# Performance work log

Measured on AMD Instinct MI355X. Metric: run time of the kernel, lower is better.

The kernel has to match this reference:

```python
import jax, jax.numpy as jnp
import numpy as np

D_EMB, D_PROJ, N_HEADS, HIDDEN = 640, 256, 4, 128
HEAD_DIM = D_PROJ // N_HEADS
B = 65536
EPS = 1e-5


def setup_inputs() -> dict:
    key = jax.random.key(0)
    ks = jax.random.split(key, 14)
    def w(k, shape, fan_in):
        return (jax.random.normal(k, shape, jnp.float32) / np.sqrt(fan_in)).astype(jnp.float32)
    return {
        "global_diff": jax.random.normal(ks[0], (B, D_EMB), jnp.float32),
        "local_diff": jax.random.normal(ks[1], (B, D_EMB), jnp.float32),
        # global/local projections ([in, out] layout; math identical to torch Linear)
        "Wg": w(ks[2], (D_EMB, D_PROJ), D_EMB), "bg": jnp.zeros((D_PROJ,), jnp.float32),
        "Wl": w(ks[3], (D_EMB, D_PROJ), D_EMB), "bl": jnp.zeros((D_PROJ,), jnp.float32),
        # MultiheadAttention packed in-proj (q|k|v) and out-proj
        "W_in": w(ks[4], (D_PROJ, 3 * D_PROJ), D_PROJ), "b_in": jnp.zeros((3 * D_PROJ,), jnp.float32),
        "W_out": w(ks[5], (D_PROJ, D_PROJ), D_PROJ), "b_out": jnp.zeros((D_PROJ,), jnp.float32),
        # LayerNorm
        "gamma": jnp.ones((D_PROJ,), jnp.float32), "beta": jnp.zeros((D_PROJ,), jnp.float32),
        # MLP head
        "W1": w(ks[6], (D_PROJ, HIDDEN), D_PROJ), "b1": jnp.zeros((HIDDEN,), jnp.float32),
        "W2": w(ks[7], (HIDDEN, 1), HIDDEN), "b2": jnp.zeros((1,), jnp.float32),
    }


def reference(global_diff, local_diff, Wg, bg, Wl, bl, W_in, b_in, W_out, b_out,
              gamma, beta, W1, b1, W2, b2):
    # projections (eval mode: dropout inactive)
    g = global_diff @ Wg + bg              # [B, P] -- the single query token
    l = local_diff @ Wl + bl               # [B, P]
    kv = jnp.stack([g, l], axis=1)         # [B, 2, P]

    Wq, Wk, Wv = jnp.split(W_in, 3, axis=1)
    bq, bk, bv = jnp.split(b_in, 3)
    b = g.shape[0]
    q = (g @ Wq + bq).reshape(b, N_HEADS, HEAD_DIM)        # [B, H, d]
    k = (kv @ Wk + bk).reshape(b, 2, N_HEADS, HEAD_DIM)    # [B, 2, H, d]
    v = (kv @ Wv + bv).reshape(b, 2, N_HEADS, HEAD_DIM)

    scale = 1.0 / np.sqrt(HEAD_DIM)
    scores = jnp.einsum('bhd,bshd->bhs', q, k) * scale     # [B, H, 2]
    attn = jax.nn.softmax(scores, axis=-1)
    ctx = jnp.einsum('bhs,bshd->bhd', attn, v).reshape(b, D_PROJ)
    attended = ctx @ W_out + b_out                         # [B, P]

    # residual + LayerNorm (eps=1e-5, torch default)
    x = g + attended
    mu = jnp.mean(x, axis=-1, keepdims=True)
    var = jnp.mean(jnp.square(x - mu), axis=-1, keepdims=True)
    y = (x - mu) * jax.lax.rsqrt(var + EPS) * gamma + beta

    # MLP head: Linear -> exact GELU (torch default) -> Linear
    h = jax.nn.gelu(y @ W1 + b1, approximate=False)
    out = (h @ W2 + b2).squeeze(-1)                        # [B]
    return out
```

## Files before the change

### kernel.cpp

```cpp
#include <hip/hip_runtime.h>
#include <math.h>

typedef __attribute__((ext_vector_type(4))) float f32x4;
typedef __attribute__((ext_vector_type(8))) __bf16 bf16x8;

static constexpr int WG_OFF = 0;
static constexpr int WL_OFF = 163840;
static constexpr int WQ_OFF = 327680;
static constexpr int WK_OFF = 393216;
static constexpr int WV_OFF = 458752;
static constexpr int WO_OFF = 524288;
static constexpr int W1_OFF = 589824;
static constexpr int W_TOTAL = 622592;

__device__ __forceinline__ unsigned short f2bf(float f) {
  unsigned u = __builtin_bit_cast(unsigned, f);
  u += 0x7FFFu + ((u >> 16) & 1u);
  return (unsigned short)(u >> 16);
}

__device__ __forceinline__ f32x4 mfma16(bf16x8 a, bf16x8 b, f32x4 c) {
  return __builtin_amdgcn_mfma_f32_16x16x32_bf16(a, b, c, 0, 0, 0);
}
__device__ __forceinline__ f32x4 fzero4() {
  f32x4 v; v[0] = 0.f; v[1] = 0.f; v[2] = 0.f; v[3] = 0.f; return v;
}

__device__ __forceinline__ bf16x8 ldB(const unsigned short* __restrict__ ws, int fragIdx, int lane) {
  return *(const bf16x8*)(ws + (size_t)(fragIdx * 64 + lane) * 8);
}

template <int STRIDE>
__device__ __forceinline__ bf16x8 ldA(const char* s, int row, int kbyte) {
  return *(const bf16x8*)(s + row * STRIDE + (kbyte ^ ((row & 7) << 4)));
}

__device__ __forceinline__ void stC(char* s, int row, int col, float v) {
  *(__bf16*)(s + row * 512 + ((col * 2) ^ ((row & 7) << 4))) = (__bf16)v;
}
__device__ __forceinline__ float ldC(const char* s, int row, int col) {
  return (float)*(const __bf16*)(s + row * 512 + ((col * 2) ^ ((row & 7) << 4)));
}

__device__ __forceinline__ bf16x8 cvt8(float4 a, float4 b) {
  bf16x8 t;
  t[0] = (__bf16)a.x; t[1] = (__bf16)a.y; t[2] = (__bf16)a.z; t[3] = (__bf16)a.w;
  t[4] = (__bf16)b.x; t[5] = (__bf16)b.y; t[6] = (__bf16)b.z; t[7] = (__bf16)b.w;
  return t;
}

template <int N>
__device__ __forceinline__ void red16(float* v) {
#pragma unroll
  for (int m = 1; m < 16; m <<= 1) {
#pragma unroll
    for (int i = 0; i < N; ++i) v[i] += __shfl_xor(v[i], m);
  }
}

__device__ __forceinline__ void stageA32(const float* __restrict__ A, char* sA, int tid) {
#pragma unroll
  for (int i = 0; i < 5; ++i) {
    const int idx = i * 512 + tid;
    const int row = idx / 80;
    const int c8 = idx - row * 80;
    const float* ap = A + (size_t)idx * 8;
    float4 f0 = *(const float4*)ap;
    float4 f1 = *(const float4*)(ap + 4);
    *(bf16x8*)(sA + row * 1280 + ((c8 * 16) ^ ((row & 7) << 4))) = cvt8(f0, f1);
  }
}

__device__ __forceinline__ void proj640(const char* sA, const unsigned short* __restrict__ wsW,
                                        const float* __restrict__ bias, char* sDst,
                                        int f0, int lane) {
  const int l15 = lane & 15, kg4 = lane >> 4;
  f32x4 acc[2][2];
#pragma unroll
  for (int m = 0; m < 2; ++m)
#pragma unroll
    for (int n = 0; n < 2; ++n) acc[m][n] = fzero4();
#pragma unroll 2
  for (int kt = 0; kt < 20; ++kt) {
    bf16x8 b0 = ldB(wsW, kt * 16 + f0, lane);
    bf16x8 b1 = ldB(wsW, kt * 16 + f0 + 1, lane);
    const int kb = kt * 64 + kg4 * 16;
#pragma unroll
    for (int m = 0; m < 2; ++m) {
      bf16x8 a = ldA<1280>(sA, m * 16 + l15, kb);
      acc[m][0] = mfma16(a, b0, acc[m][0]);
      acc[m][1] = mfma16(a, b1, acc[m][1]);
    }
  }
#pragma unroll
  for (int n = 0; n < 2; ++n) {
    const int col = (f0 + n) * 16 + l15;
    const float bv = bias[col];
#pragma unroll
    for (int m = 0; m < 2; ++m)
#pragma unroll
      for (int r = 0; r < 4; ++r)
        stC(sDst, m * 16 + kg4 * 4 + r, col, acc[m][n][r] + bv);
  }
}

__device__ __forceinline__ void gemm256(const char* sA, const unsigned short* __restrict__ wsW,
                                        int f0, f32x4 (&acc)[2][2], int lane) {
  const int l15 = lane & 15, kg4 = lane >> 4;
#pragma unroll 2
  for (int kt = 0; kt < 8; ++kt) {
    bf16x8 b0 = ldB(wsW, kt * 16 + f0, lane);
    bf16x8 b1 = ldB(wsW, kt * 16 + f0 + 1, lane);
    const int kb = kt * 64 + kg4 * 16;
#pragma unroll
    for (int m = 0; m < 2; ++m) {
      bf16x8 a = ldA<512>(sA, m * 16 + l15, kb);
      acc[m][0] = mfma16(a, b0, acc[m][0]);
      acc[m][1] = mfma16(a, b1, acc[m][1]);
    }
  }
}

__device__ __forceinline__ void gemm256d(const char* sG, const char* sL,
                                         const unsigned short* __restrict__ wsW, int f0,
                                         f32x4 (&ag)[2][2], f32x4 (&al)[2][2], int lane) {
  const int l15 = lane & 15, kg4 = lane >> 4;
#pragma unroll 2
  for (int kt = 0; kt < 8; ++kt) {
    bf16x8 b0 = ldB(wsW, kt * 16 + f0, lane);
    bf16x8 b1 = ldB(wsW, kt * 16 + f0 + 1, lane);
    const int kb = kt * 64 + kg4 * 16;
#pragma unroll
    for (int m = 0; m < 2; ++m) {
      bf16x8 g = ldA<512>(sG, m * 16 + l15, kb);
      bf16x8 l = ldA<512>(sL, m * 16 + l15, kb);
      ag[m][0] = mfma16(g, b0, ag[m][0]);
      ag[m][1] = mfma16(g, b1, ag[m][1]);
      al[m][0] = mfma16(l, b0, al[m][0]);
      al[m][1] = mfma16(l, b1, al[m][1]);
    }
  }
}

__global__ void convert_w(const float* __restrict__ Wg, const float* __restrict__ Wl,
                          const float* __restrict__ Win, const float* __restrict__ Wout,
                          const float* __restrict__ W1, unsigned short* __restrict__ ws) {
  const int tid = blockIdx.x * 256 + threadIdx.x;
  if (tid >= W_TOTAL) return;
  const float* src;
  int stride, coloff, base, lognf;
  if (tid < WL_OFF)      { src = Wg;   stride = 256; coloff = 0;   base = WG_OFF; lognf = 4; }
  else if (tid < WQ_OFF) { src = Wl;   stride = 256; coloff = 0;   base = WL_OFF; lognf = 4; }
  else if (tid < WK_OFF) { src = Win;  stride = 768; coloff = 0;   base = WQ_OFF; lognf = 4; }
  else if (tid < WV_OFF) { src = Win;  stride = 768; coloff = 256; base = WK_OFF; lognf = 4; }
  else if (tid < WO_OFF) { src = Win;  stride = 768; coloff = 512; base = WV_OFF; lognf = 4; }
  else if (tid < W1_OFF) { src = Wout; stride = 256; coloff = 0;   base = WO_OFF; lognf = 4; }
  else                   { src = W1;   stride = 128; coloff = 0;   base = W1_OFF; lognf = 3; }
  const int idx = tid - base;
  const int j = idx & 7;
  const int lane = (idx >> 3) & 63;
  const int fl = idx >> 9;
  const int n = fl & ((1 << lognf) - 1);
  const int kt = fl >> lognf;
  const int k = kt * 32 + (lane >> 4) * 8 + j;
  const int col = coloff + n * 16 + (lane & 15);
  ws[tid] = f2bf(src[k * stride + col]);
}

__global__ __launch_bounds__(512)
__attribute__((amdgpu_waves_per_eu(4, 4)))
void dca_fused(
    const float* __restrict__ gdiff, const float* __restrict__ ldiff,
    const float* __restrict__ bg, const float* __restrict__ bl,
    const float* __restrict__ bin, const float* __restrict__ bout,
    const float* __restrict__ gamma, const float* __restrict__ beta,
    const float* __restrict__ b1, const float* __restrict__ W2,
    const float* __restrict__ b2, const unsigned short* __restrict__ wsw,
    float* __restrict__ out) {
  __shared__ __align__(16) char sMem[73728];
  char* sA = sMem;
  char* sG = sMem + 40960;
  char* sL = sMem + 57344;
  float* sSc = (float*)sMem;
  float* sLN = (float*)(sMem + 2048);
  float* sMu = (float*)(sMem + 4096);
  float* sPO = (float*)(sMem + 4352);
  char* sQ = sMem + 8192;

  const int tid = threadIdx.x;
  const int blk = blockIdx.x;
  const int lane = tid & 63, l15 = lane & 15, kg4 = lane >> 4;
  const int w = tid >> 6;
  const int f0 = w * 2;

  stageA32(gdiff + (size_t)blk * 32 * 640, sA, tid);
  __syncthreads();
  proj640(sA, wsw + WG_OFF, bg, sG, f0, lane);
  __syncthreads();
  stageA32(ldiff + (size_t)blk * 32 * 640, sA, tid);
  __syncthreads();
  proj640(sA, wsw + WL_OFF, bl, sL, f0, lane);
  __syncthreads();

  {
    f32x4 qa[2][2];
#pragma unroll
    for (int m = 0; m < 2; ++m) { qa[m][0] = fzero4(); qa[m][1] = fzero4(); }
    gemm256(sG, wsw + WQ_OFF, f0, qa, lane);
#pragma unroll
    for (int m = 0; m < 2; ++m) {
      bf16x8 t;
#pragma unroll
      for (int n = 0; n < 2; ++n) {
        const float bv = bin[(f0 + n) * 16 + l15];
#pragma unroll
        for (int r = 0; r < 4; ++r) t[n * 4 + r] = (__bf16)(qa[m][n][r] + bv);
      }
      *(bf16x8*)(sQ + m * 8192 + tid * 16) = t;
    }
  }

  float s[16];
  {
    f32x4 kg[2][2], kl[2][2];
#pragma unroll
    for (int m = 0; m < 2; ++m) {
      kg[m][0] = fzero4(); kg[m][1] = fzero4();
      kl[m][0] = fzero4(); kl[m][1] = fzero4();
    }
    gemm256d(sG, sL, wsw + WK_OFF, f0, kg, kl, lane);
#pragma unroll
    for (int m = 0; m < 2; ++m) {
      bf16x8 t = *(const bf16x8*)(sQ + m * 8192 + tid * 16);
#pragma unroll
      for (int r = 0; r < 4; ++r) {
        s[m * 4 + r] = (float)t[r] * kg[m][0][r] + (float)t[4 + r] * kg[m][1][r];
        s[8 + m * 4 + r] = (float)t[r] * kl[m][0][r] + (float)t[4 + r] * kl[m][1][r];
      }
    }
  }
  red16<16>(s);
  if (l15 < 2) {
#pragma unroll
    for (int r = 0; r < 4; ++r) {
      const int row = l15 * 16 + kg4 * 4 + r;
      sSc[(w * 32 + row) * 2 + 0] = s[l15 * 4 + r];
      sSc[(w * 32 + row) * 2 + 1] = s[8 + l15 * 4 + r];
    }
  }
  __syncthreads();
  float a1v[2][4];
  {
    const int pw = w ^ 1;
#pragma unroll
    for (int m = 0; m < 2; ++m)
#pragma unroll
      for (int r = 0; r < 4; ++r) {
        const int row = m * 16 + kg4 * 4 + r;
        const float t0 = s[m * 4 + r] + sSc[(pw * 32 + row) * 2 + 0];
        const float t1 = s[8 + m * 4 + r] + sSc[(pw * 32 + row) * 2 + 1];
        a1v[m][r] = 1.0f / (1.0f + expf((t0 - t1) * 0.125f));
      }
  }

  f32x4 ctx[2][2];
  {
    f32x4 vg[2][2], vl[2][2];
#pragma unroll
    for (int m = 0; m < 2; ++m) {
      vg[m][0] = fzero4(); vg[m][1] = fzero4();
      vl[m][0] = fzero4(); vl[m][1] = fzero4();
    }
    gemm256d(sG, sL, wsw + WV_OFF, f0, vg, vl, lane);
#pragma unroll
    for (int n = 0; n < 2; ++n) {
      const float bv = bin[512 + (f0 + n) * 16 + l15];
#pragma unroll
      for (int m = 0; m < 2; ++m)
#pragma unroll
        for (int r = 0; r < 4; ++r)
          ctx[m][n][r] = (1.0f - a1v[m][r]) * vg[m][n][r] + a1v[m][r] * vl[m][n][r] + bv;
    }
  }
  __syncthreads();
#pragma unroll
  for (int n = 0; n < 2; ++n) {
    const int col = (f0 + n) * 16 + l15;
#pragma unroll
    for (int m = 0; m < 2; ++m)
#pragma unroll
      for (int r = 0; r < 4; ++r)
        stC(sL, m * 16 + kg4 * 4 + r, col, ctx[m][n][r]);
  }
  __syncthreads();

  {
    f32x4 at[2][2];
#pragma unroll
    for (int m = 0; m < 2; ++m) { at[m][0] = fzero4(); at[m][1] = fzero4(); }
    gemm256(sL, wsw + WO_OFF, f0, at, lane);
    float st[16];
#pragma unroll
    for (int i = 0; i < 16; ++i) st[i] = 0.f;
#pragma unroll
    for (int n = 0; n < 2; ++n) {
      const int col = (f0 + n) * 16 + l15;
      const float bv = bout[col];
#pragma unroll
      for (int m = 0; m < 2; ++m)
#pragma unroll
        for (int r = 0; r < 4; ++r) {
          const int row = m * 16 + kg4 * 4 + r;
          const float x = at[m][n][r] + bv + ldC(sG, row, col);
          stC(sG, row, col, x);
          st[m * 4 + r] += x;
          st[8 + m * 4 + r] += x * x;
        }
    }
    red16<16>(st);
    if (l15 < 2) {
#pragma unroll
      for (int r = 0; r < 4; ++r) {
        const int row = l15 * 16 + kg4 * 4 + r;
        sLN[(w * 32 + row) * 2 + 0] = st[l15 * 4 + r];
        sLN[(w * 32 + row) * 2 + 1] = st[8 + l15 * 4 + r];
      }
    }
  }
  __syncthreads();
  if (tid < 64) {
    const int row = tid >> 1, j = tid & 1;
    float v = 0.f;
#pragma unroll
    for (int ww = 0; ww < 8; ++ww) v += sLN[(ww * 32 + row) * 2 + j];
    sMu[row * 2 + j] = v;
  }
  __syncthreads();
#pragma unroll
  for (int n = 0; n < 2; ++n) {
    const int col = (f0 + n) * 16 + l15;
    const float ga = gamma[col], be = beta[col];
#pragma unroll
    for (int m = 0; m < 2; ++m)
#pragma unroll
      for (int r = 0; r < 4; ++r) {
        const int row = m * 16 + kg4 * 4 + r;
        const float m_ = sMu[row * 2 + 0] * (1.0f / 256.0f);
        const float var = sMu[row * 2 + 1] * (1.0f / 256.0f) - m_ * m_;
        const float x = ldC(sG, row, col);
        stC(sG, row, col, (x - m_) * rsqrtf(var + 1e-5f) * ga + be);
      }
  }
  __syncthreads();

  f32x4 ha[2];
  ha[0] = fzero4();
  ha[1] = fzero4();
#pragma unroll 2
  for (int kt = 0; kt < 8; ++kt) {
    bf16x8 b = ldB(wsw + W1_OFF, kt * 8 + w, lane);
    const int kb = kt * 64 + kg4 * 16;
#pragma unroll
    for (int m = 0; m < 2; ++m) {
      bf16x8 a = ldA<512>(sG, m * 16 + l15, kb);
      ha[m] = mfma16(a, b, ha[m]);
    }
  }
  {
    const int colh = w * 16 + l15;
    const float bv1 = b1[colh], w2v = W2[colh];
    float o[8];
#pragma unroll
    for (int m = 0; m < 2; ++m)
#pragma unroll
      for (int r = 0; r < 4; ++r) {
        float hv = ha[m][r] + bv1;
        hv = 0.5f * hv * (1.0f + erff(hv * 0.70710678118654752f));
        o[m * 4 + r] = hv * w2v;
      }
    red16<8>(o);
    if (l15 < 2) {
#pragma unroll
      for (int r = 0; r < 4; ++r)
        sPO[w * 32 + l15 * 16 + kg4 * 4 + r] = o[l15 * 4 + r];
    }
  }
  __syncthreads();
  if (tid < 32) {
    float acc = b2[0];
#pragma unroll
    for (int ww = 0; ww < 8; ++ww) acc += sPO[ww * 32 + tid];
    out[(size_t)blk * 32 + tid] = acc;
  }
}

extern "C" void kernel_launch(void* const* d_in, const int* in_sizes, int n_in,
                              void* d_out, int out_size, void* d_ws, size_t ws_size,
                              hipStream_t stream) {
  (void)in_sizes; (void)n_in; (void)out_size; (void)ws_size;
  const float* gdiff = (const float*)d_in[0];
  const float* ldiff = (const float*)d_in[1];
  const float* Wg    = (const float*)d_in[2];
  const float* bg    = (const float*)d_in[3];
  const float* Wl    = (const float*)d_in[4];
  const float* bl    = (const float*)d_in[5];
  const float* Win   = (const float*)d_in[6];
  const float* bin   = (const float*)d_in[7];
  const float* Wout  = (const float*)d_in[8];
  const float* bout  = (const float*)d_in[9];
  const float* gamma = (const float*)d_in[10];
  const float* beta  = (const float*)d_in[11];
  const float* W1    = (const float*)d_in[12];
  const float* b1    = (const float*)d_in[13];
  const float* W2    = (const float*)d_in[14];
  const float* b2    = (const float*)d_in[15];
  unsigned short* ws = (unsigned short*)d_ws;
  float* out = (float*)d_out;

  convert_w<<<dim3((W_TOTAL + 255) / 256), dim3(256), 0, stream>>>(Wg, Wl, Win, Wout, W1, ws);
  dca_fused<<<dim3(2048), dim3(512), 0, stream>>>(gdiff, ldiff, bg, bl, bin, bout, gamma,
                                                  beta, b1, W2, b2,
                                                  (const unsigned short*)ws, out);
}
```

Baseline: 207.9 us.

## Process 64 rows per block with 16 waves each owning one column tile

Doubles the rows per workgroup from 32 to 64 and the threads from 512 to 1024. Each wave now owns a single 16-wide output column tile across four row tiles instead of two column tiles across two row tiles, so each weight fragment loaded from global memory is reused over more rows. Attention score and LayerNorm reductions are reworked into a two-level cross-wave reduction through shared memory. LDS use doubles to 144KB, which allows only one block per CU and may reduce latency hiding. The extra reduction pass adds barriers.

```diff
diff --git a/kernel.cpp b/kernel.cpp
--- a/kernel.cpp
+++ b/kernel.cpp
@@ -58,10 +58,10 @@
   }
 }
 
-__device__ __forceinline__ void stageA32(const float* __restrict__ A, char* sA, int tid) {
+__device__ __forceinline__ void stageA64(const float* __restrict__ A, char* sA, int tid) {
 #pragma unroll
   for (int i = 0; i < 5; ++i) {
-    const int idx = i * 512 + tid;
+    const int idx = i * 1024 + tid;
     const int row = idx / 80;
     const int c8 = idx - row * 80;
     const float* ap = A + (size_t)idx * 8;
@@ -71,73 +71,61 @@
   }
 }
 
-__device__ __forceinline__ void proj640(const char* sA, const unsigned short* __restrict__ wsW,
-                                        const float* __restrict__ bias, char* sDst,
-                                        int f0, int lane) {
+__device__ __forceinline__ void proj640w(const char* sA, const unsigned short* __restrict__ wsW,
+                                         const float* __restrict__ bias, char* sDst,
+                                         int w, int lane) {
   const int l15 = lane & 15, kg4 = lane >> 4;
-  f32x4 acc[2][2];
-#pragma unroll
-  for (int m = 0; m < 2; ++m)
-#pragma unroll
-    for (int n = 0; n < 2; ++n) acc[m][n] = fzero4();
+  f32x4 acc[4];
+#pragma unroll
+  for (int m = 0; m < 4; ++m) acc[m] = fzero4();
 #pragma unroll 2
   for (int kt = 0; kt < 20; ++kt) {
-    bf16x8 b0 = ldB(wsW, kt * 16 + f0, lane);
-    bf16x8 b1 = ldB(wsW, kt * 16 + f0 + 1, lane);
+    bf16x8 b = ldB(wsW, kt * 16 + w, lane);
     const int kb = kt * 64 + kg4 * 16;
 #pragma unroll
-    for (int m = 0; m < 2; ++m) {
+    for (int m = 0; m < 4; ++m) {
       bf16x8 a = ldA<1280>(sA, m * 16 + l15, kb);
-      acc[m][0] = mfma16(a, b0, acc[m][0]);
-      acc[m][1] = mfma16(a, b1, acc[m][1]);
-    }
-  }
-#pragma unroll
-  for (int n = 0; n < 2; ++n) {
-    const int col = (f0 + n) * 16 + l15;
-    const float bv = bias[col];
-#pragma unroll
-    for (int m = 0; m < 2; ++m)
-#pragma unroll
-      for (int r = 0; r < 4; ++r)
-        stC(sDst, m * 16 + kg4 * 4 + r, col, acc[m][n][r] + bv);
-  }
-}
-
-__device__ __forceinline__ void gemm256(const char* sA, const unsigned short* __restrict__ wsW,
-                                        int f0, f32x4 (&acc)[2][2], int lane) {
+      acc[m] = mfma16(a, b, acc[m]);
+    }
+  }
+  const int col = w * 16 + l15;
+  const float bv = bias[col];
+#pragma unroll
+  for (int m = 0; m < 4; ++m)
+#pragma unroll
+    for (int r = 0; r < 4; ++r)
+      stC(sDst, m * 16 + kg4 * 4 + r, col, acc[m][r] + bv);
+}
+
+__device__ __forceinline__ void gemm256w(const char* sA, const unsigned short* __restrict__ wsW,
+                                         int w, f32x4 (&acc)[4], int lane) {
   const int l15 = lane & 15, kg4 = lane >> 4;
 #pragma unroll 2
   for (int kt = 0; kt < 8; ++kt) {
-    bf16x8 b0 = ldB(wsW, kt * 16 + f0, lane);
-    bf16x8 b1 = ldB(wsW, kt * 16 + f0 + 1, lane);
+    bf16x8 b = ldB(wsW, kt * 16 + w, lane);
     const int kb = kt * 64 + kg4 * 16;
 #pragma unroll
-    for (int m = 0; m < 2; ++m) {
+    for (int m = 0; m < 4; ++m) {
       bf16x8 a = ldA<512>(sA, m * 16 + l15, kb);
-      acc[m][0] = mfma16(a, b0, acc[m][0]);
-      acc[m][1] = mfma16(a, b1, acc[m][1]);
-    }
-  }
-}
-
-__device__ __forceinline__ void gemm256d(const char* sG, const char* sL,
-                                         const unsigned short* __restrict__ wsW, int f0,
-                                         f32x4 (&ag)[2][2], f32x4 (&al)[2][2], int lane) {
+      acc[m] = mfma16(a, b, acc[m]);
+    }
+  }
+}
+
+__device__ __forceinline__ void gemm256dw(const char* sG, const char* sL,
+                                          const unsigned short* __restrict__ wsW, int w,
+                                          f32x4 (&ag)[4], f32x4 (&al)[4], int lane) {
   const int l15 = lane & 15, kg4 = lane >> 4;
 #pragma unroll 2
   for (int kt = 0; kt < 8; ++kt) {
-    bf16x8 b0 = ldB(wsW, kt * 16 + f0, lane);
-    bf16x8 b1 = ldB(wsW, kt * 16 + f0 + 1, lane);
+    bf16x8 b = ldB(wsW, kt * 16 + w, lane);
     const int kb = kt * 64 + kg4 * 16;
 #pragma unroll
-    for (int m = 0; m < 2; ++m) {
+    for (int m = 0; m < 4; ++m) {
       bf16x8 g = ldA<512>(sG, m * 16 + l15, kb);
       bf16x8 l = ldA<512>(sL, m * 16 + l15, kb);
-      ag[m][0] = mfma16(g, b0, ag[m][0]);
-      ag[m][1] = mfma16(g, b1, ag[m][1]);
-      al[m][0] = mfma16(l, b0, al[m][0]);
-      al[m][1] = mfma16(l, b1, al[m][1]);
+      ag[m] = mfma16(g, b, ag[m]);
+      al[m] = mfma16(l, b, al[m]);
     }
   }
 }
@@ -167,7 +155,7 @@
   ws[tid] = f2bf(src[k * stride + col]);
 }
 
-__global__ __launch_bounds__(512)
+__global__ __launch_bounds__(1024)
 __attribute__((amdgpu_waves_per_eu(4, 4)))
 void dca_fused(
     const float* __restrict__ gdiff, const float* __restrict__ ldiff,
@@ -177,171 +165,173 @@
     const float* __restrict__ b1, const float* __restrict__ W2,
     const float* __restrict__ b2, const unsigned short* __restrict__ wsw,
     float* __restrict__ out) {
-  __shared__ __align__(16) char sMem[73728];
+  __shared__ __align__(16) char sMem[147456];
   char* sA = sMem;
-  char* sG = sMem + 40960;
-  char* sL = sMem + 57344;
-  float* sSc = (float*)sMem;
-  float* sLN = (float*)(sMem + 2048);
-  float* sMu = (float*)(sMem + 4096);
-  float* sPO = (float*)(sMem + 4352);
-  char* sQ = sMem + 8192;
+  char* sG = sMem + 81920;
+  char* sL = sMem + 114688;
+  char* sQ = sMem;
+  float* sSc = (float*)(sMem + 32768);
+  float* sScR = (float*)(sMem + 40960);
+  float* sLN = (float*)(sMem + 43008);
+  float* sMu = (float*)(sMem + 51200);
+  float* sPO = (float*)(sMem + 51712);
 
   const int tid = threadIdx.x;
   const int blk = blockIdx.x;
   const int lane = tid & 63, l15 = lane & 15, kg4 = lane >> 4;
   const int w = tid >> 6;
-  const int f0 = w * 2;
-
-  stageA32(gdiff + (size_t)blk * 32 * 640, sA, tid);
-  __syncthreads();
-  proj640(sA, wsw + WG_OFF, bg, sG, f0, lane);
-  __syncthreads();
-  stageA32(ldiff + (size_t)blk * 32 * 640, sA, tid);
-  __syncthreads();
-  proj640(sA, wsw + WL_OFF, bl, sL, f0, lane);
-  __syncthreads();
-
-  {
-    f32x4 qa[2][2];
-#pragma unroll
-    for (int m = 0; m < 2; ++m) { qa[m][0] = fzero4(); qa[m][1] = fzero4(); }
-    gemm256(sG, wsw + WQ_OFF, f0, qa, lane);
-#pragma unroll
-    for (int m = 0; m < 2; ++m) {
-      bf16x8 t;
-#pragma unroll
-      for (int n = 0; n < 2; ++n) {
-        const float bv = bin[(f0 + n) * 16 + l15];
-#pragma unroll
-        for (int r = 0; r < 4; ++r) t[n * 4 + r] = (__bf16)(qa[m][n][r] + bv);
-      }
-      *(bf16x8*)(sQ + m * 8192 + tid * 16) = t;
-    }
-  }
-
-  float s[16];
-  {
-    f32x4 kg[2][2], kl[2][2];
-#pragma unroll
-    for (int m = 0; m < 2; ++m) {
-      kg[m][0] = fzero4(); kg[m][1] = fzero4();
-      kl[m][0] = fzero4(); kl[m][1] = fzero4();
-    }
-    gemm256d(sG, sL, wsw + WK_OFF, f0, kg, kl, lane);
-#pragma unroll
-    for (int m = 0; m < 2; ++m) {
-      bf16x8 t = *(const bf16x8*)(sQ + m * 8192 + tid * 16);
-#pragma unroll
-      for (int r = 0; r < 4; ++r) {
-        s[m * 4 + r] = (float)t[r] * kg[m][0][r] + (float)t[4 + r] * kg[m][1][r];
-        s[8 + m * 4 + r] = (float)t[r] * kl[m][0][r] + (float)t[4 + r] * kl[m][1][r];
-      }
-    }
-  }
-  red16<16>(s);
-  if (l15 < 2) {
+
+  stageA64(gdiff + (size_t)blk * 64 * 640, sA, tid);
+  __syncthreads();
+  proj640w(sA, wsw + WG_OFF, bg, sG, w, lane);
+  __syncthreads();
+  stageA64(ldiff + (size_t)blk * 64 * 640, sA, tid);
+  __syncthreads();
+  proj640w(sA, wsw + WL_OFF, bl, sL, w, lane);
+  __syncthreads();
+
+  {
+    f32x4 qa[4];
+#pragma unroll
+    for (int m = 0; m < 4; ++m) qa[m] = fzero4();
+    gemm256w(sG, wsw + WQ_OFF, w, qa, lane);
+    const float bv = bin[w * 16 + l15];
+    bf16x8 t0, t1;
 #pragma unroll
     for (int r = 0; r < 4; ++r) {
-      const int row = l15 * 16 + kg4 * 4 + r;
-      sSc[(w * 32 + row) * 2 + 0] = s[l15 * 4 + r];
-      sSc[(w * 32 + row) * 2 + 1] = s[8 + l15 * 4 + r];
-    }
-  }
-  __syncthreads();
-  float a1v[2][4];
-  {
-    const int pw = w ^ 1;
-#pragma unroll
-    for (int m = 0; m < 2; ++m)
+      t0[r] = (__bf16)(qa[0][r] + bv);
+      t0[4 + r] = (__bf16)(qa[1][r] + bv);
+      t1[r] = (__bf16)(qa[2][r] + bv);
+      t1[4 + r] = (__bf16)(qa[3][r] + bv);
+    }
+    *(bf16x8*)(sQ + tid * 32) = t0;
+    *(bf16x8*)(sQ + tid * 32 + 16) = t1;
+  }
+
+  float s[32];
+  {
+    f32x4 kg[4], kl[4];
+#pragma unroll
+    for (int m = 0; m < 4; ++m) { kg[m] = fzero4(); kl[m] = fzero4(); }
+    gemm256dw(sG, sL, wsw + WK_OFF, w, kg, kl, lane);
+    bf16x8 t0 = *(const bf16x8*)(sQ + tid * 32);
+    bf16x8 t1 = *(const bf16x8*)(sQ + tid * 32 + 16);
+#pragma unroll
+    for (int m = 0; m < 4; ++m)
+#pragma unroll
+      for (int r = 0; r < 4; ++r) {
+        const float qv = (m < 2) ? (float)t0[m * 4 + r] : (float)t1[(m - 2) * 4 + r];
+        s[m * 4 + r] = qv * kg[m][r];
+        s[16 + m * 4 + r] = qv * kl[m][r];
+      }
+  }
+  red16<32>(s);
+  if (l15 == 0) {
+#pragma unroll
+    for (int m = 0; m < 4; ++m)
 #pragma unroll
       for (int r = 0; r < 4; ++r) {
         const int row = m * 16 + kg4 * 4 + r;
-        const float t0 = s[m * 4 + r] + sSc[(pw * 32 + row) * 2 + 0];
-        const float t1 = s[8 + m * 4 + r] + sSc[(pw * 32 + row) * 2 + 1];
+        sSc[(w * 64 + row) * 2 + 0] = s[m * 4 + r];
+        sSc[(w * 64 + row) * 2 + 1] = s[16 + m * 4 + r];
+      }
+  }
+  __syncthreads();
+  if (tid < 128) {
+    const int row = tid >> 1, j = tid & 1;
+#pragma unroll
+    for (int h = 0; h < 4; ++h) {
+      float v = 0.f;
+#pragma unroll
+      for (int i = 0; i < 4; ++i) v += sSc[((h * 4 + i) * 64 + row) * 2 + j];
+      sScR[(row * 4 + h) * 2 + j] = v;
+    }
+  }
+  __syncthreads();
+  float a1v[4][4];
+  {
+    const int head = w >> 2;
+#pragma unroll
+    for (int m = 0; m < 4; ++m)
+#pragma unroll
+      for (int r = 0; r < 4; ++r) {
+        const int row = m * 16 + kg4 * 4 + r;
+        const float t0 = sScR[(row * 4 + head) * 2 + 0];
+        const float t1 = sScR[(row * 4 + head) * 2 + 1];
         a1v[m][r] = 1.0f / (1.0f + expf((t0 - t1) * 0.125f));
       }
   }
 
-  f32x4 ctx[2][2];
-  {
-    f32x4 vg[2][2], vl[2][2];
-#pragma unroll
-    for (int m = 0; m < 2; ++m) {
-      vg[m][0] = fzero4(); vg[m][1] = fzero4();
-      vl[m][0] = fzero4(); vl[m][1] = fzero4();
-    }
-    gemm256d(sG, sL, wsw + WV_OFF, f0, vg, vl, lane);
-#pragma unroll
-    for (int n = 0; n < 2; ++n) {
-      const float bv = bin[512 + (f0 + n) * 16 + l15];
-#pragma unroll
-      for (int m = 0; m < 2; ++m)
-#pragma unroll
-        for (int r = 0; r < 4; ++r)
-          ctx[m][n][r] = (1.0f - a1v[m][r]) * vg[m][n][r] + a1v[m][r] * vl[m][n][r] + bv;
-    }
-  }
-  __syncthreads();
-#pragma unroll
-  for (int n = 0; n < 2; ++n) {
-    const int col = (f0 + n) * 16 + l15;
-#pragma unroll
-    for (int m = 0; m < 2; ++m)
+  f32x4 ctx[4];
+  {
+    f32x4 vg[4], vl[4];
+#pragma unroll
+    for (int m = 0; m < 4; ++m) { vg[m] = fzero4(); vl[m] = fzero4(); }
+    gemm256dw(sG, sL, wsw + WV_OFF, w, vg, vl, lane);
+    const float bv = bin[512 + w * 16 + l15];
+#pragma unroll
+    for (int m = 0; m < 4; ++m)
 #pragma unroll
       for (int r = 0; r < 4; ++r)
-        stC(sL, m * 16 + kg4 * 4 + r, col, ctx[m][n][r]);
-  }
-  __syncthreads();
-
-  {
-    f32x4 at[2][2];
-#pragma unroll
-    for (int m = 0; m < 2; ++m) { at[m][0] = fzero4(); at[m][1] = fzero4(); }
-    gemm256(sL, wsw + WO_OFF, f0, at, lane);
-    float st[16];
-#pragma unroll
-    for (int i = 0; i < 16; ++i) st[i] = 0.f;
-#pragma unroll
-    for (int n = 0; n < 2; ++n) {
-      const int col = (f0 + n) * 16 + l15;
-      const float bv = bout[col];
-#pragma unroll
-      for (int m = 0; m < 2; ++m)
+        ctx[m][r] = (1.0f - a1v[m][r]) * vg[m][r] + a1v[m][r] * vl[m][r] + bv;
+  }
+  __syncthreads();
+  {
+    const int col = w * 16 + l15;
+#pragma unroll
+    for (int m = 0; m < 4; ++m)
+#pragma unroll
+      for (int r = 0; r < 4; ++r)
+        stC(sL, m * 16 + kg4 * 4 + r, col, ctx[m][r]);
+  }
+  __syncthreads();
+
+  {
+    f32x4 at[4];
+#pragma unroll
+    for (int m = 0; m < 4; ++m) at[m] = fzero4();
+    gemm256w(sL, wsw + WO_OFF, w, at, lane);
+    float st[32];
+#pragma unroll
+    for (int i = 0; i < 32; ++i) st[i] = 0.f;
+    const int col = w * 16 + l15;
+    const float bv = bout[col];
+#pragma unroll
+    for (int m = 0; m < 4; ++m)
+#pragma unroll
+      for (int r = 0; r < 4; ++r) {
+        const int row = m * 16 + kg4 * 4 + r;
+        const float x = at[m][r] + bv + ldC(sG, row, col);
+        stC(sG, row, col, x);
+        st[m * 4 + r] = x;
+        st[16 + m * 4 + r] = x * x;
+      }
+    red16<32>(st);
+    if (l15 == 0) {
+#pragma unroll
+      for (int m = 0; m < 4; ++m)
 #pragma unroll
         for (int r = 0; r < 4; ++r) {
           const int row = m * 16 + kg4 * 4 + r;
-          const float x = at[m][n][r] + bv + ldC(sG, row, col);
-          stC(sG, row, col, x);
-          st[m * 4 + r] += x;
-          st[8 + m * 4 + r] += x * x;
+          sLN[(w * 64 + row) * 2 + 0] = st[m * 4 + r];
+          sLN[(w * 64 + row) * 2 + 1] = st[16 + m * 4 + r];
         }
     }
-    red16<16>(st);
-    if (l15 < 2) {
-#pragma unroll
-      for (int r = 0; r < 4; ++r) {
-        const int row = l15 * 16 + kg4 * 4 + r;
-        sLN[(w * 32 + row) * 2 + 0] = st[l15 * 4 + r];
-        sLN[(w * 32 + row) * 2 + 1] = st[8 + l15 * 4 + r];
-      }
-    }
-  }
-  __syncthreads();
-  if (tid < 64) {
+  }
+  __syncthreads();
+  if (tid < 128) {
     const int row = tid >> 1, j = tid & 1;
     float v = 0.f;
 #pragma unroll
-    for (int ww = 0; ww < 8; ++ww) v += sLN[(ww * 32 + row) * 2 + j];
+    for (int ww = 0; ww < 16; ++ww) v += sLN[(ww * 64 + row) * 2 + j];
     sMu[row * 2 + j] = v;
   }
   __syncthreads();
-#pragma unroll
-  for (int n = 0; n < 2; ++n) {
-    const int col = (f0 + n) * 16 + l15;
+  {
+    const int col = w * 16 + l15;
     const float ga = gamma[col], be = beta[col];
 #pragma unroll
-    for (int m = 0; m < 2; ++m)
+    for (int m = 0; m < 4; ++m)
 #pragma unroll
       for (int r = 0; r < 4; ++r) {
         const int row = m * 16 + kg4 * 4 + r;
@@ -353,44 +343,47 @@
   }
   __syncthreads();
 
-  f32x4 ha[2];
-  ha[0] = fzero4();
-  ha[1] = fzero4();
+  {
+    const int fr = w & 7, mb = (w >> 3) * 2;
+    f32x4 ha[2];
+    ha[0] = fzero4();
+    ha[1] = fzero4();
 #pragma unroll 2
-  for (int kt = 0; kt < 8; ++kt) {
-    bf16x8 b = ldB(wsw + W1_OFF, kt * 8 + w, lane);
-    const int kb = kt * 64 + kg4 * 16;
-#pragma unroll
-    for (int m = 0; m < 2; ++m) {
-      bf16x8 a = ldA<512>(sG, m * 16 + l15, kb);
-      ha[m] = mfma16(a, b, ha[m]);
-    }
-  }
-  {
-    const int colh = w * 16 + l15;
+    for (int kt = 0; kt < 8; ++kt) {
+      bf16x8 b = ldB(wsw + W1_OFF, kt * 8 + fr, lane);
+      const int kb = kt * 64 + kg4 * 16;
+#pragma unroll
+      for (int mm = 0; mm < 2; ++mm) {
+        bf16x8 a = ldA<512>(sG, (mb + mm) * 16 + l15, kb);
+        ha[mm] = mfma16(a, b, ha[mm]);
+      }
+    }
+    const int colh = fr * 16 + l15;
     const float bv1 = b1[colh], w2v = W2[colh];
     float o[8];
 #pragma unroll
-    for (int m = 0; m < 2; ++m)
-#pragma unroll
-      for (int r = 0; r < 4; ++r) {
-        float hv = ha[m][r] + bv1;
+    for (int mm = 0; mm < 2; ++mm)
+#pragma unroll
+      for (int r = 0; r < 4; ++r) {
+        float hv = ha[mm][r] + bv1;
         hv = 0.5f * hv * (1.0f + erff(hv * 0.70710678118654752f));
-        o[m * 4 + r] = hv * w2v;
+        o[mm * 4 + r] = hv * w2v;
       }
     red16<8>(o);
-    if (l15 < 2) {
-#pragma unroll
-      for (int r = 0; r < 4; ++r)
-        sPO[w * 32 + l15 * 16 + kg4 * 4 + r] = o[l15 * 4 + r];
-    }
-  }
-  __syncthreads();
-  if (tid < 32) {
+    if (l15 == 0) {
+#pragma unroll
+      for (int mm = 0; mm < 2; ++mm)
+#pragma unroll
+        for (int r = 0; r < 4; ++r)
+          sPO[fr * 64 + (mb + mm) * 16 + kg4 * 4 + r] = o[mm * 4 + r];
+    }
+  }
+  __syncthreads();
+  if (tid < 64) {
     float acc = b2[0];
 #pragma unroll
-    for (int ww = 0; ww < 8; ++ww) acc += sPO[ww * 32 + tid];
-    out[(size_t)blk * 32 + tid] = acc;
+    for (int f = 0; f < 8; ++f) acc += sPO[f * 64 + tid];
+    out[(size_t)blk * 64 + tid] = acc;
   }
 }
 
@@ -418,7 +411,7 @@
   float* out = (float*)d_out;
 
   convert_w<<<dim3((W_TOTAL + 255) / 256), dim3(256), 0, stream>>>(Wg, Wl, Win, Wout, W1, ws);
-  dca_fused<<<dim3(2048), dim3(512), 0, stream>>>(gdiff, ldiff, bg, bl, bin, bout, gamma,
-                                                  beta, b1, W2, b2,
-                                                  (const unsigned short*)ws, out);
-}
+  dca_fused<<<dim3(1024), dim3(1024), 0, stream>>>(gdiff, ldiff, bg, bl, bin, bout, gamma,
+                                                   beta, b1, W2, b2,
+                                                   (const unsigned short*)ws, out);
+}
```

Measured after the change: 252.9 us. 1.22x slower.
